# Performance work log

Measured on AMD Instinct MI355X. Metric: run time of the kernel, lower is better.

The kernel has to match this reference:

```python
import jax, jax.numpy as jnp
import numpy as np
from functools import partial

B, S, D_IN, H = 8, 2048, 1024, 1024
V = 50257
NUM_CODEWORDS, EMB_DIM = 256, 16
NUM_NEURONS, TOP_K = 64, 16  # top_k = sparsity(0.25) * 64
TILE_ROWS = 16
NUM_TILES = H // TILE_ROWS  # 64 -> decoder out_features = 1024
FREQS = (1.0, 2.0, 4.0)
MAX_LEN = 1024


def setup_inputs() -> dict:
    key = jax.random.key(0)
    ks = jax.random.split(key, 16)
    s = 0.02
    return {
        "inputs": jax.random.normal(ks[0], (B, S, D_IN), jnp.float32),
        "Wt": jax.random.normal(ks[1], (H, D_IN), jnp.float32) * s,
        "bt": jnp.zeros((H,), jnp.float32),
        "Wq": jax.random.normal(ks[2], (H, H), jnp.float32) * s,
        "bq": jnp.zeros((H,), jnp.float32),
        "Wk": jax.random.normal(ks[3], (H, H), jnp.float32) * s,
        "bk": jnp.zeros((H,), jnp.float32),
        "Wv": jax.random.normal(ks[4], (H, H), jnp.float32) * s,
        "bv": jnp.zeros((H,), jnp.float32),
        "Wo": jax.random.normal(ks[5], (D_IN, H), jnp.float32) * s,
        "bo": jnp.zeros((D_IN,), jnp.float32),
        "codebook": jax.random.normal(ks[6], (NUM_CODEWORDS, EMB_DIM), jnp.float32) * s,
        "instructions": jax.random.randint(ks[7], (NUM_TILES * TILE_ROWS, D_IN // EMB_DIM), 0, NUM_CODEWORDS),
        "W_lm": jax.random.normal(ks[8], (V, NUM_TILES * TILE_ROWS), jnp.float32) * s,
        "b_lm": jnp.zeros((V,), jnp.float32),
    }


def _positional_bias(seq_len):
    # AttentionBasisSynthesizer: sin/cos atoms at freqs (1,2,4), gains=1, shifts=0
    ang = 2.0 * jnp.pi * jnp.arange(seq_len, dtype=jnp.float32) / MAX_LEN
    bias = jnp.zeros((seq_len,), jnp.float32)
    for f in FREQS:
        bias = bias + jnp.sin(f * ang) + jnp.cos(f * ang)
    return bias  # [S]


def _forward(inputs, Wt, bt, Wq, bq, Wk, bk, Wv, bv, Wo, bo, codebook, instructions, W_lm, b_lm):
    tokens = inputs @ Wt.T + bt                       # [B,S,H]
    q = tokens @ Wq.T + bq
    k = tokens @ Wk.T + bk
    v = tokens @ Wv.T + bv
    # per-step KV-cache loop == causal attention over prefix; vectorize
    scores = jnp.einsum("bqh,bkh->bqk", q, k) / jnp.sqrt(jnp.float32(H))
    scores = scores + _positional_bias(S)[None, None, :]
    i = jnp.arange(S)
    causal = i[:, None] >= i[None, :]                 # [S,S]
    scores = jnp.where(causal[None], scores, -jnp.inf)
    attn = jnp.einsum("bqk,bkh->bqh", jax.nn.softmax(scores, axis=-1), v)  # [B,S,H]
    # sparse routing: group into NUM_NEURONS neurons, keep top-k by L2 norm,
    # softmax weights over kept neurons, straight-through combine with dense path
    g = attn.reshape(B, S, NUM_NEURONS, H // NUM_NEURONS)
    sc = jnp.sqrt(jnp.sum(g * g, axis=-1))            # [B,S,N]
    vals, idx = jax.lax.top_k(sc, TOP_K)              # [B,S,K]
    w = jax.nn.softmax(vals, axis=-1)
    onehot = jax.nn.one_hot(idx, NUM_NEURONS, dtype=attn.dtype)  # [B,S,K,N]
    wfull = jnp.einsum("bsk,bskn->bsn", w, onehot)    # [B,S,N]
    combined = (g * wfull[..., None]).reshape(B, S, H)
    combined = combined + (attn - jax.lax.stop_gradient(attn))  # straight-through
    dec_in = combined @ Wo.T + bo                     # [B,S,D_IN]
    x = jnp.mean(dec_in, axis=1)                      # [B,D_IN]
    # DemopackDecoder: weight rows assembled from codebook via instruction indices
    W_dec = codebook[instructions].reshape(NUM_TILES * TILE_ROWS, D_IN)
    hidden = x @ W_dec.T                              # [B, 1024]
    return hidden @ W_lm.T + b_lm                     # [B, V]


def reference(inputs, Wt, bt, Wq, bq, Wk, bk, Wv, bv, Wo, bo, codebook, instructions, W_lm, b_lm):
    return _forward(inputs, Wt, bt, Wq, bq, Wk, bk, Wv, bv, Wo, bo, codebook, instructions, W_lm, b_lm)
```

## Files before the change

### kernel.cpp

```cpp
#include <hip/hip_runtime.h>
#include <cstdint>
#include <cstddef>

#define B_   8
#define S_   2048
#define DIN_ 1024
#define H_   1024
#define V_   50257

typedef unsigned short ushort_t;
typedef __bf16 bf16x8 __attribute__((ext_vector_type(8)));
typedef float  f32x4  __attribute__((ext_vector_type(4)));

__device__ __forceinline__ ushort_t f2bf(float x) {
    unsigned u = __float_as_uint(x);
    u = (u + 0x7fffu + ((u >> 16) & 1u)) >> 16;
    return (ushort_t)u;
}

__device__ __forceinline__ void async16(const void* g, void* s) {
    __builtin_amdgcn_global_load_lds(
        (const __attribute__((address_space(1))) unsigned int*)g,
        (__attribute__((address_space(3))) unsigned int*)s, 16, 0, 0);
}

__device__ __forceinline__ float wredmax(float v) {
#pragma unroll
    for (int o = 32; o; o >>= 1) v = fmaxf(v, __shfl_xor(v, o));
    return v;
}
__device__ __forceinline__ float wredsum(float v) {
#pragma unroll
    for (int o = 32; o; o >>= 1) v += __shfl_xor(v, o);
    return v;
}

#define NB0 16384
#define NB1 19456
#define NB2 19712
#define NB3 20480
#define NB4 20488
__global__ __launch_bounds__(256)
void setup_all(const float* __restrict__ inputs,
               const float* __restrict__ Wq, const float* __restrict__ Wk,
               const float* __restrict__ Wv, const float* __restrict__ Wt,
               const float* __restrict__ bq, const float* __restrict__ bk,
               const float* __restrict__ bv, const float* __restrict__ bt,
               ushort_t* __restrict__ inbf, ushort_t* __restrict__ wqkv_bf,
               ushort_t* __restrict__ wtT, float* __restrict__ bcomb,
               float* __restrict__ pbias) {
    __shared__ float twt[64][65];
    int blk = blockIdx.x, tid = threadIdx.x;
    if (blk < NB0) {
        int i = blk * 256 + tid;
        float4 f = ((const float4*)inputs)[i];
        ushort4 u;
        u.x = f2bf(f.x); u.y = f2bf(f.y); u.z = f2bf(f.z); u.w = f2bf(f.w);
        ((ushort4*)inbf)[i] = u;
    } else if (blk < NB1) {
        int i = (blk - NB0) * 256 + tid;
        int w = i >> 18, off = i & 262143;
        const float* src = w == 0 ? Wq : (w == 1 ? Wk : Wv);
        float4 f = ((const float4*)src)[off];
        ushort4 u;
        u.x = f2bf(f.x); u.y = f2bf(f.y); u.z = f2bf(f.z); u.w = f2bf(f.w);
        ((ushort4*)(wqkv_bf + (size_t)w * 1048576))[off] = u;
    } else if (blk < NB2) {
        int j = blk - NB1;
        int k0 = (j & 15) * 64, i0 = (j >> 4) * 64;
        int tx = tid & 63, ty = tid >> 6;
#pragma unroll
        for (int jj = 0; jj < 16; jj++) {
            int k = ty * 16 + jj;
            twt[k][tx] = Wt[(size_t)(k0 + k) * DIN_ + i0 + tx];
        }
        __syncthreads();
#pragma unroll
        for (int jj = 0; jj < 16; jj++) {
            int i = ty * 16 + jj;
            wtT[(size_t)(i0 + i) * H_ + k0 + tx] = f2bf(twt[tx][i]);
        }
    } else if (blk < NB3) {
        int wave = tid >> 6, lane = tid & 63;
        int j = (blk - NB2) * 4 + wave;
        const float* W  = j < 1024 ? Wq : (j < 2048 ? Wk : Wv);
        const float* bb = j < 1024 ? bq : (j < 2048 ? bk : bv);
        int rowj = j & 1023;
        const float4* wr4 = (const float4*)(W + (size_t)rowj * 1024);
        const float4* bt4 = (const float4*)bt;
        float s = 0.f;
#pragma unroll
        for (int c = 0; c < 4; c++) {
            float4 w = wr4[c * 64 + lane];
            float4 b = bt4[c * 64 + lane];
            s += w.x * b.x + w.y * b.y + w.z * b.z + w.w * b.w;
        }
        s = wredsum(s);
        if (lane == 0) bcomb[j] = s + bb[rowj];
    } else {
        int k = (blk - NB3) * 256 + tid;
        float ang = 6.283185307179586f * (float)k / 1024.0f;
        float b = 0.f;
        b += sinf(1.f * ang) + cosf(1.f * ang);
        b += sinf(2.f * ang) + cosf(2.f * ang);
        b += sinf(4.f * ang) + cosf(4.f * ang);
        pbias[k] = b;
    }
}

template <int OUT_BF16>
__global__ __launch_bounds__(256)
void gemm_bt(const ushort_t* __restrict__ A, int lda,
             const ushort_t* __restrict__ Bt, int ldb,
             void* __restrict__ Cv, int ldc, int K, const float* __restrict__ bias) {
    int bn = blockIdx.x, bm = blockIdx.y;
    __shared__ ushort_t As[128 * 32];
    __shared__ ushort_t Bs[128 * 32];
    int tid = threadIdx.x, wave = tid >> 6, lane = tid & 63;
    int wr = wave >> 1, wc = wave & 1;
    int nkt = K >> 5;
    int srow = lane >> 2, scol = (lane & 3) * 8;
    size_t arow0 = (size_t)bm * 128, brow0 = (size_t)bn * 128;
    f32x4 acc[4][4];
#pragma unroll
    for (int m = 0; m < 4; m++)
#pragma unroll
        for (int n = 0; n < 4; n++) acc[m][n] = f32x4{0.f, 0.f, 0.f, 0.f};
    for (int kt = 0; kt < nkt; ++kt) {
        int k0 = kt * 32;
#pragma unroll
        for (int i = 0; i < 2; i++) {
            int reg = wave * 2 + i;
            int row = reg * 16 + srow;
            async16(A + (arow0 + row) * (size_t)lda + k0 + scol, (ushort_t*)As + reg * 512);
            async16(Bt + (brow0 + row) * (size_t)ldb + k0 + scol, (ushort_t*)Bs + reg * 512);
        }
        __syncthreads();
        bf16x8 af[4], bfr[4];
#pragma unroll
        for (int m = 0; m < 4; m++)
            af[m] = *(const bf16x8*)&As[(wr * 64 + m * 16 + (lane & 15)) * 32 + (lane >> 4) * 8];
#pragma unroll
        for (int n = 0; n < 4; n++)
            bfr[n] = *(const bf16x8*)&Bs[(wc * 64 + n * 16 + (lane & 15)) * 32 + (lane >> 4) * 8];
#pragma unroll
        for (int m = 0; m < 4; m++)
#pragma unroll
            for (int n = 0; n < 4; n++)
                acc[m][n] = __builtin_amdgcn_mfma_f32_16x16x32_bf16(af[m], bfr[n], acc[m][n], 0, 0, 0);
        __syncthreads();
    }
    int rl = (lane >> 4) * 4, cl = lane & 15;
#pragma unroll
    for (int m = 0; m < 4; m++)
#pragma unroll
        for (int n = 0; n < 4; n++) {
            int col = bn * 128 + wc * 64 + n * 16 + cl;
            float badd = bias ? bias[col] : 0.f;
#pragma unroll
            for (int r = 0; r < 4; r++) {
                int row = bm * 128 + wr * 64 + m * 16 + rl + r;
                float v = acc[m][n][r] + badd;
                size_t off = (size_t)row * ldc + col;
                if (OUT_BF16) ((ushort_t*)Cv)[off] = f2bf(v);
                else          ((float*)Cv)[off] = v;
            }
        }
}

template <int OUT_BF16, int MODE>
__global__ __launch_bounds__(512, 2)
void gemm256(const ushort_t* __restrict__ A, size_t sAb, int lda,
             const ushort_t* __restrict__ Bt, size_t sBb, int ldb,
             void* __restrict__ Cv, size_t sCb, int ldc,
             int K, const float* __restrict__ bias, int nbn, int nwg,
             float* __restrict__ Cv2) {
    extern __shared__ char lds[];
    int bz = blockIdx.y;
    int bm, bn, koff = 0, nkt;
    void* Cuse = Cv;
    size_t sCuse = sCb;
    if (MODE == 2) {
        int x = blockIdx.x;
        if (x < 32) {
            bm = x >> 2; bn = x & 3;
            int km = (bm + 1) * 256; if (km > 1024) km = 1024;
            nkt = km >> 6;
        } else {
            int j = x - 32;
            bm = 7 - (j >> 2); bn = j & 3;
            koff = 1024;
            nkt = ((bm + 1) * 256 - 1024) >> 6;
            Cuse = Cv2;
            sCuse = (size_t)1024 * 1024;
        }
    } else if (MODE == 1) {
        int orig = blockIdx.x;
        if (orig >= 36) {
            ushort_t (*t)[66] = (ushort_t(*)[66])lds;
            ushort_t* vT = (ushort_t*)Cv2;
            const ushort_t* qkvp = A;
            int j = orig - 36;
            int tx = threadIdx.x & 63, ty = threadIdx.x >> 6;
            for (int rep = 0; rep < 8; rep++) {
                int tile = j * 8 + rep;
                int s0 = (tile & 31) * 64, h0 = (tile >> 5) * 64;
#pragma unroll
                for (int i = 0; i < 8; i++) {
                    int s = ty * 8 + i;
                    t[s][tx] = qkvp[((size_t)bz * S_ + s0 + s) * 3072 + 2048 + h0 + tx];
                }
                __syncthreads();
#pragma unroll
                for (int i = 0; i < 8; i++) {
                    int h = ty * 8 + i;
                    vT[((size_t)bz * H_ + h0 + h) * S_ + s0 + tx] = t[tx][h];
                }
                __syncthreads();
            }
            return;
        }
        int qq = 36 >> 3, rr8 = 36 & 7;
        int xcd = orig & 7, bidx = orig >> 3;
        int wgid = (xcd < rr8 ? xcd * (qq + 1) : rr8 * (qq + 1) + (xcd - rr8) * qq) + bidx;
        int w = wgid;
        bm = 0;
        while ((bm + 1) * (bm + 2) / 2 <= w) bm++;
        bn = w - bm * (bm + 1) / 2;
        nkt = K >> 6;
    } else {
        int orig = blockIdx.x;
        int qq = nwg >> 3, rr8 = nwg & 7;
        int xcd = orig & 7, bidx = orig >> 3;
        int wgid = (xcd < rr8 ? xcd * (qq + 1) : rr8 * (qq + 1) + (xcd - rr8) * qq) + bidx;
        bm = wgid / nbn; bn = wgid - bm * nbn;
        nkt = K >> 6;
    }

    const ushort_t* Ab = A + (size_t)bz * sAb;
    const ushort_t* Bb = Bt + (size_t)bz * sBb;
    int tid = threadIdx.x, wave = tid >> 6, lane = tid & 63;
    int wr = wave >> 2, wc = wave & 3;

    int srow = wave * 8 + (lane >> 3);
    int sswz = ((lane & 7) ^ (lane >> 3)) * 8;
    const ushort_t* Ag = Ab + ((size_t)bm * 256 + srow) * (size_t)lda + sswz + koff;
    const ushort_t* Bg = Bb + ((size_t)bn * 256 + srow) * (size_t)ldb + sswz + koff;
    int sdst = wave * 1024;

    int fr = lane & 15, g = lane >> 4;
    int kx = (fr >> 2) & 1;
    int gsw = (g ^ (fr & 3)) * 16;
    int aoff = wr * 16384 + fr * 128 + gsw;
    int boff = 32768 + (wc >> 1) * 16384 + ((wc & 1) * 64 + fr) * 128 + gsw;
    int ks0 = kx << 6, ks1 = (kx ^ 1) << 6;

    f32x4 acc[8][4];
#pragma unroll
    for (int m = 0; m < 8; m++)
#pragma unroll
        for (int n = 0; n < 4; n++) acc[m][n] = f32x4{0.f, 0.f, 0.f, 0.f};

#define STG_A(t, h, bo)                                                        \
    do {                                                                       \
        async16(Ag + (size_t)((h) * 128) * lda + (t) * 64,                     \
                lds + (bo) + (h) * 16384 + sdst);                              \
        async16(Ag + (size_t)((h) * 128 + 64) * lda + (t) * 64,                \
                lds + (bo) + (h) * 16384 + 8192 + sdst);                       \
    } while (0)
#define STG_B(t, h, bo)                                                        \
    do {                                                                       \
        async16(Bg + (size_t)((h) * 128) * ldb + (t) * 64,                     \
                lds + (bo) + 32768 + (h) * 16384 + sdst);                      \
        async16(Bg + (size_t)((h) * 128 + 64) * ldb + (t) * 64,                \
                lds + (bo) + 32768 + (h) * 16384 + 8192 + sdst);               \
    } while (0)

    STG_A(0, 0, 0); STG_A(0, 1, 0); STG_B(0, 0, 0); STG_B(0, 1, 0);
    STG_A(1, 0, 65536); STG_A(1, 1, 65536); STG_B(1, 0, 65536); STG_B(1, 1, 65536);
    asm volatile("s_waitcnt vmcnt(8)" ::: "memory");
    __builtin_amdgcn_sched_barrier(0);
    __builtin_amdgcn_s_barrier();
    __builtin_amdgcn_sched_barrier(0);

    bf16x8 af03[4][2], af47[4][2], bf01[2][2], bf23[2][2];
#pragma unroll
    for (int mf = 0; mf < 4; mf++) {
        af03[mf][0] = *(const bf16x8*)(lds + aoff + mf * 2048 + ks0);
        af03[mf][1] = *(const bf16x8*)(lds + aoff + mf * 2048 + ks1);
    }
#pragma unroll
    for (int nf = 0; nf < 2; nf++) {
        bf01[nf][0] = *(const bf16x8*)(lds + boff + nf * 2048 + ks0);
        bf01[nf][1] = *(const bf16x8*)(lds + boff + nf * 2048 + ks1);
    }

    int bufo = 0;
    for (int t = 0; t < nkt; ++t, bufo ^= 65536) {
        int nb = bufo ^ 65536;
#pragma unroll
        for (int mf = 0; mf < 4; mf++) {
            af47[mf][0] = *(const bf16x8*)(lds + bufo + aoff + (mf + 4) * 2048 + ks0);
            af47[mf][1] = *(const bf16x8*)(lds + bufo + aoff + (mf + 4) * 2048 + ks1);
        }
        __builtin_amdgcn_s_setprio(1);
#pragma unroll
        for (int mf = 0; mf < 4; mf++)
#pragma unroll
            for (int nf = 0; nf < 2; nf++) {
                acc[mf][nf] = __builtin_amdgcn_mfma_f32_16x16x32_bf16(af03[mf][0], bf01[nf][0], acc[mf][nf], 0, 0, 0);
                acc[mf][nf] = __builtin_amdgcn_mfma_f32_16x16x32_bf16(af03[mf][1], bf01[nf][1], acc[mf][nf], 0, 0, 0);
            }
        __builtin_amdgcn_s_setprio(0);
        __builtin_amdgcn_sched_barrier(0);
        asm volatile("s_waitcnt lgkmcnt(0)" ::: "memory");
        __builtin_amdgcn_sched_barrier(0);
        __builtin_amdgcn_s_barrier();
        __builtin_amdgcn_sched_barrier(0);

#pragma unroll
        for (int nf = 0; nf < 2; nf++) {
            bf23[nf][0] = *(const bf16x8*)(lds + bufo + boff + (nf + 2) * 2048 + ks0);
            bf23[nf][1] = *(const bf16x8*)(lds + bufo + boff + (nf + 2) * 2048 + ks1);
        }
        __builtin_amdgcn_s_setprio(1);
#pragma unroll
        for (int mf = 0; mf < 4; mf++)
#pragma unroll
            for (int nf = 0; nf < 2; nf++) {
                acc[mf + 4][nf] = __builtin_amdgcn_mfma_f32_16x16x32_bf16(af47[mf][0], bf01[nf][0], acc[mf + 4][nf], 0, 0, 0);
                acc[mf + 4][nf] = __builtin_amdgcn_mfma_f32_16x16x32_bf16(af47[mf][1], bf01[nf][1], acc[mf + 4][nf], 0, 0, 0);
            }
        __builtin_amdgcn_s_setprio(0);
        __builtin_amdgcn_sched_barrier(0);
        __builtin_amdgcn_s_barrier();
        __builtin_amdgcn_sched_barrier(0);

        if (t + 2 < nkt) STG_A(t + 2, 0, bufo);
        __builtin_amdgcn_s_setprio(1);
#pragma unroll
        for (int mf = 0; mf < 4; mf++)
#pragma unroll
            for (int nf = 0; nf < 2; nf++) {
                acc[mf][nf + 2] = __builtin_amdgcn_mfma_f32_16x16x32_bf16(af03[mf][0], bf23[nf][0], acc[mf][nf + 2], 0, 0, 0);
                acc[mf][nf + 2] = __builtin_amdgcn_mfma_f32_16x16x32_bf16(af03[mf][1], bf23[nf][1], acc[mf][nf + 2], 0, 0, 0);
            }
        __builtin_amdgcn_s_setprio(0);
        __builtin_amdgcn_sched_barrier(0);
        if (t + 1 < nkt) {
            if (t + 2 < nkt) { asm volatile("s_waitcnt vmcnt(2)" ::: "memory"); }
            else             { asm volatile("s_waitcnt vmcnt(0)" ::: "memory"); }
        }
        __builtin_amdgcn_s_barrier();
        __builtin_amdgcn_sched_barrier(0);

        if (t + 1 < nkt) {
#pragma unroll
            for (int mf = 0; mf < 4; mf++) {
                af03[mf][0] = *(const bf16x8*)(lds + nb + aoff + mf * 2048 + ks0);
                af03[mf][1] = *(const bf16x8*)(lds + nb + aoff + mf * 2048 + ks1);
            }
#pragma unroll
            for (int nf = 0; nf < 2; nf++) {
                bf01[nf][0] = *(const bf16x8*)(lds + nb + boff + nf * 2048 + ks0);
                bf01[nf][1] = *(const bf16x8*)(lds + nb + boff + nf * 2048 + ks1);
            }
        }
        if (t + 2 < nkt) { STG_A(t + 2, 1, bufo); STG_B(t + 2, 0, bufo); STG_B(t + 2, 1, bufo); }
        __builtin_amdgcn_s_setprio(1);
#pragma unroll
        for (int mf = 0; mf < 4; mf++)
#pragma unroll
            for (int nf = 0; nf < 2; nf++) {
                acc[mf + 4][nf + 2] = __builtin_amdgcn_mfma_f32_16x16x32_bf16(af47[mf][0], bf23[nf][0], acc[mf + 4][nf + 2], 0, 0, 0);
                acc[mf + 4][nf + 2] = __builtin_amdgcn_mfma_f32_16x16x32_bf16(af47[mf][1], bf23[nf][1], acc[mf + 4][nf + 2], 0, 0, 0);
            }
        __builtin_amdgcn_s_setprio(0);
        __builtin_amdgcn_sched_barrier(0);
        __builtin_amdgcn_s_barrier();
        __builtin_amdgcn_sched_barrier(0);
    }
#undef STG_A
#undef STG_B

    int rl = (lane >> 4) * 4, cl = lane & 15;
#pragma unroll
    for (int mf = 0; mf < 8; mf++)
#pragma unroll
        for (int nf = 0; nf < 4; nf++) {
            int col = bn * 256 + wc * 64 + nf * 16 + cl;
            float badd = bias ? bias[col] : 0.f;
#pragma unroll
            for (int r = 0; r < 4; r++) {
                int row = bm * 256 + wr * 128 + mf * 16 + rl + r;
                float v = acc[mf][nf][r] + badd;
                size_t off = (size_t)bz * sCuse + (size_t)row * ldc + col;
                if (OUT_BF16) ((ushort_t*)Cuse)[off] = f2bf(v);
                else          ((float*)Cuse)[off] = v;
            }
        }
}

__global__ __launch_bounds__(256)
void softmax_kernel(const float* __restrict__ scores, ushort_t* __restrict__ P,
                    const float* __restrict__ bias) {
    __shared__ float red[8];
    int q = blockIdx.x, b = blockIdx.y;
    int L = q + 1;
    int tid = threadIdx.x;
    const float4* srow4 = (const float4*)(scores + ((size_t)b * S_ + q) * S_);
    const float4* bias4 = (const float4*)bias;
    const float scale = 0.03125f;
    int kz = ((q >> 8) + 1) * 256;

    int k00 = tid * 4, k01 = 1024 + tid * 4;
    float4 v0 = {0.f, 0.f, 0.f, 0.f}, v1 = {0.f, 0.f, 0.f, 0.f};
    float lm = -3e38f;
    if (k00 < kz) {
        float4 s4 = srow4[tid];
        float4 b4 = bias4[tid];
        v0.x = (k00 + 0 < L) ? s4.x * scale + b4.x : -3e38f;
        v0.y = (k00 + 1 < L) ? s4.y * scale + b4.y : -3e38f;
        v0.z = (k00 + 2 < L) ? s4.z * scale + b4.z : -3e38f;
        v0.w = (k00 + 3 < L) ? s4.w * scale + b4.w : -3e38f;
        lm = fmaxf(fmaxf(v0.x, v0.y), fmaxf(v0.z, v0.w));
    }
    if (k01 < kz) {
        float4 s4 = srow4[256 + tid];
        float4 b4 = bias4[256 + tid];
        v1.x = (k01 + 0 < L) ? s4.x * scale + b4.x : -3e38f;
        v1.y = (k01 + 1 < L) ? s4.y * scale + b4.y : -3e38f;
        v1.z = (k01 + 2 < L) ? s4.z * scale + b4.z : -3e38f;
        v1.w = (k01 + 3 < L) ? s4.w * scale + b4.w : -3e38f;
        lm = fmaxf(lm, fmaxf(fmaxf(v1.x, v1.y), fmaxf(v1.z, v1.w)));
    }
    lm = wredmax(lm);
    if ((tid & 63) == 0) red[tid >> 6] = lm;
    __syncthreads();
    float m = fmaxf(fmaxf(red[0], red[1]), fmaxf(red[2], red[3]));

    float ls = 0.f;
    if (k00 < kz) {
        v0.x = __expf(v0.x - m); v0.y = __expf(v0.y - m);
        v0.z = __expf(v0.z - m); v0.w = __expf(v0.w - m);
        ls += v0.x + v0.y + v0.z + v0.w;
    }
    if (k01 < kz) {
        v1.x = __expf(v1.x - m); v1.y = __expf(v1.y - m);
        v1.z = __expf(v1.z - m); v1.w = __expf(v1.w - m);
        ls += v1.x + v1.y + v1.z + v1.w;
    }
    ls = wredsum(ls);
    if ((tid & 63) == 0) red[4 + (tid >> 6)] = ls;
    __syncthreads();
    float invs = 1.f / (red[4] + red[5] + red[6] + red[7]);

    ushort_t* prow = P + ((size_t)b * S_ + q) * S_;
    if (k00 < kz) {
        ushort4 o;
        o.x = f2bf(v0.x * invs); o.y = f2bf(v0.y * invs);
        o.z = f2bf(v0.z * invs); o.w = f2bf(v0.w * invs);
        ((ushort4*)prow)[tid] = o;
    }
    if (k01 < kz) {
        ushort4 o;
        o.x = f2bf(v1.x * invs); o.y = f2bf(v1.y * invs);
        o.z = f2bf(v1.z * invs); o.w = f2bf(v1.w * invs);
        ((ushort4*)prow)[256 + tid] = o;
    }
}

__global__ __launch_bounds__(256)
void routing_kernel(const float* __restrict__ attn, const float* __restrict__ attn2,
                    ushort_t* __restrict__ combined) {
    int wave = threadIdx.x >> 6, lane = threadIdx.x & 63;
    size_t row = (size_t)blockIdx.x * 4 + wave;
    const float4* a4 = (const float4*)(attn + row * H_);
    float4 x0 = a4[lane * 4 + 0], x1 = a4[lane * 4 + 1];
    float4 x2 = a4[lane * 4 + 2], x3 = a4[lane * 4 + 3];
    int q = (int)(row & 2047);
    if (q >= 1024) {
        size_t b = row >> 11;
        const float4* a2 = (const float4*)(attn2 + ((b * 1024 + (size_t)(q - 1024)) * H_));
        float4 y0 = a2[lane * 4 + 0], y1 = a2[lane * 4 + 1];
        float4 y2 = a2[lane * 4 + 2], y3 = a2[lane * 4 + 3];
        x0.x += y0.x; x0.y += y0.y; x0.z += y0.z; x0.w += y0.w;
        x1.x += y1.x; x1.y += y1.y; x1.z += y1.z; x1.w += y1.w;
        x2.x += y2.x; x2.y += y2.y; x2.z += y2.z; x2.w += y2.w;
        x3.x += y3.x; x3.y += y3.y; x3.z += y3.z; x3.w += y3.w;
    }
    float ss = x0.x * x0.x + x0.y * x0.y + x0.z * x0.z + x0.w * x0.w
             + x1.x * x1.x + x1.y * x1.y + x1.z * x1.z + x1.w * x1.w
             + x2.x * x2.x + x2.y * x2.y + x2.z * x2.z + x2.w * x2.w
             + x3.x * x3.x + x3.y * x3.y + x3.z * x3.z + x3.w * x3.w;
    float sc = sqrtf(ss);

    float v = sc, thr = 0.f, mx = 0.f;
#pragma unroll
    for (int i = 0; i < 16; i++) {
        float mm = wredmax(v);
        if (i == 0) mx = mm;
        thr = mm;
        if (v == mm) v = -1e30f;
    }
    float e = (sc >= thr) ? __expf(sc - mx) : 0.f;
    float se = wredsum(e);
    float w = e / se;

    const float xs[16] = {x0.x, x0.y, x0.z, x0.w, x1.x, x1.y, x1.z, x1.w,
                          x2.x, x2.y, x2.z, x2.w, x3.x, x3.y, x3.z, x3.w};
    union { ushort_t u[16]; uint4 q4[2]; } pk;
#pragma unroll
    for (int j = 0; j < 16; j++) pk.u[j] = f2bf(xs[j] * w);
    uint4* dst = (uint4*)(combined + row * H_ + lane * 16);
    dst[0] = pk.q4[0];
    dst[1] = pk.q4[1];
}

__global__ void cmean_part(const ushort_t* __restrict__ comb, float* __restrict__ part) {
    int d = blockIdx.x * 256 + threadIdx.x;
    int sc = blockIdx.y, b = blockIdx.z;
    const ushort_t* p = comb + ((size_t)b * S_ + sc * 128) * H_ + d;
    float s = 0.f;
    for (int i = 0; i < 128; i++) s += __uint_as_float((unsigned)p[(size_t)i * H_] << 16);
    part[((size_t)b * 16 + sc) * H_ + d] = s;
}

__global__ void cmean_final(const float* __restrict__ part, float* __restrict__ cm) {
    int idx = blockIdx.x * 256 + threadIdx.x;
    int b = idx >> 10, d = idx & 1023;
    float s = 0.f;
#pragma unroll
    for (int c = 0; c < 16; c++) s += part[((size_t)b * 16 + c) * DIN_ + d];
    cm[idx] = s * (1.0f / 2048.0f);
}

__global__ __launch_bounds__(256)
void xgemv(const float* __restrict__ cm, const float* __restrict__ Wo,
           const float* __restrict__ bo, float* __restrict__ x) {
    int wave = threadIdx.x >> 6, lane = threadIdx.x & 63;
    int i = blockIdx.x * 4 + wave;
    const float4* wr4 = (const float4*)(Wo + (size_t)i * H_);
    float4 w[4];
#pragma unroll
    for (int c = 0; c < 4; c++) w[c] = wr4[c * 64 + lane];
    float accv[B_];
#pragma unroll
    for (int b = 0; b < B_; b++) {
        const float4* c4 = (const float4*)(cm + (size_t)b * H_);
        float s = 0.f;
#pragma unroll
        for (int c = 0; c < 4; c++) {
            float4 h = c4[c * 64 + lane];
            s += w[c].x * h.x + w[c].y * h.y + w[c].z * h.z + w[c].w * h.w;
        }
        accv[b] = wredsum(s);
    }
    if (lane == 0) {
        float bi = bo[i];
#pragma unroll
        for (int b = 0; b < B_; b++) x[(size_t)b * DIN_ + i] = accv[b] + bi;
    }
}

__global__ __launch_bounds__(64)
void decode_hidden(const float* __restrict__ x, const float* __restrict__ codebook,
                   const int* __restrict__ instr, float* __restrict__ hidden) {
    int r = blockIdx.x;
    int lane = threadIdx.x;
    int idx = instr[r * 64 + lane];
    const float4* cw = (const float4*)(codebook + (size_t)idx * 16);
    float4 c0 = cw[0], c1 = cw[1], c2 = cw[2], c3 = cw[3];
    float acc[B_];
#pragma unroll
    for (int b = 0; b < B_; b++) {
        const float4* xb = (const float4*)(x + (size_t)b * DIN_ + lane * 16);
        float4 h0 = xb[0], h1 = xb[1], h2 = xb[2], h3 = xb[3];
        acc[b] = c0.x * h0.x + c0.y * h0.y + c0.z * h0.z + c0.w * h0.w
               + c1.x * h1.x + c1.y * h1.y + c1.z * h1.z + c1.w * h1.w
               + c2.x * h2.x + c2.y * h2.y + c2.z * h2.z + c2.w * h2.w
               + c3.x * h3.x + c3.y * h3.y + c3.z * h3.z + c3.w * h3.w;
    }
#pragma unroll
    for (int b = 0; b < B_; b++) acc[b] = wredsum(acc[b]);
    if (lane == 0) {
#pragma unroll
        for (int b = 0; b < B_; b++) hidden[(size_t)b * 1024 + r] = acc[b];
    }
}

__global__ __launch_bounds__(256)
void lm_head(const float* __restrict__ Wlm, const float* __restrict__ hidden,
             const float* __restrict__ blm, float* __restrict__ out) {
    int wave = threadIdx.x >> 6, lane = threadIdx.x & 63;
    for (int v = blockIdx.x * 4 + wave; v < V_; v += gridDim.x * 4) {
        const float4* wrow = (const float4*)(Wlm + (size_t)v * 1024);
        float acc[B_];
#pragma unroll
        for (int b = 0; b < B_; b++) acc[b] = 0.f;
#pragma unroll
        for (int rr = 0; rr < 4; rr++) {
            float4 wv = wrow[rr * 64 + lane];
#pragma unroll
            for (int b = 0; b < B_; b++) {
                float4 hv = ((const float4*)hidden)[b * 256 + rr * 64 + lane];
                acc[b] += wv.x * hv.x + wv.y * hv.y + wv.z * hv.z + wv.w * hv.w;
            }
        }
#pragma unroll
        for (int b = 0; b < B_; b++) acc[b] = wredsum(acc[b]);
        if (lane == 0) {
            float bl = blm[v];
#pragma unroll
            for (int b = 0; b < B_; b++) out[(size_t)b * V_ + v] = acc[b] + bl;
        }
    }
}

extern "C" void kernel_launch(void* const* d_in, const int* in_sizes, int n_in,
                              void* d_out, int out_size, void* d_ws, size_t ws_size,
                              hipStream_t stream) {
    const float* inputs = (const float*)d_in[0];
    const float* Wt  = (const float*)d_in[1];
    const float* bt  = (const float*)d_in[2];
    const float* Wq  = (const float*)d_in[3];
    const float* bq  = (const float*)d_in[4];
    const float* Wk  = (const float*)d_in[5];
    const float* bk  = (const float*)d_in[6];
    const float* Wv  = (const float*)d_in[7];
    const float* bv  = (const float*)d_in[8];
    const float* Wo  = (const float*)d_in[9];
    const float* bo  = (const float*)d_in[10];
    const float* codebook = (const float*)d_in[11];
    const int*   instructions = (const int*)d_in[12];
    const float* Wlm = (const float*)d_in[13];
    const float* blm = (const float*)d_in[14];
    float* out = (float*)d_out;

    (void)hipFuncSetAttribute(reinterpret_cast<const void*>(&gemm256<1, 0>),
                              hipFuncAttributeMaxDynamicSharedMemorySize, 131072);
    (void)hipFuncSetAttribute(reinterpret_cast<const void*>(&gemm256<0, 1>),
                              hipFuncAttributeMaxDynamicSharedMemorySize, 131072);
    (void)hipFuncSetAttribute(reinterpret_cast<const void*>(&gemm256<0, 2>),
                              hipFuncAttributeMaxDynamicSharedMemorySize, 131072);

    const size_t MB = 1024 * 1024;
    char* ws = (char*)d_ws;
    ushort_t* wqkv_bf = (ushort_t*)(ws + 0);
    ushort_t* wtT_bf  = (ushort_t*)(ws + 6 * MB);
    ushort_t* wcomb   = (ushort_t*)(ws + 8 * MB);
    float* bcomb  = (float*)(ws + 14 * MB);
    float* pbias  = (float*)(ws + 14 * MB + 64 * 1024);
    float* cm     = (float*)(ws + 14 * MB + 128 * 1024);
    float* xbuf   = (float*)(ws + 14 * MB + 192 * 1024);
    float* hidden = (float*)(ws + 14 * MB + 256 * 1024);
    float* part   = (float*)(ws + 14 * MB + 512 * 1024);
    ushort_t* inbf   = (ushort_t*)(ws + 16 * MB);
    ushort_t* qkv    = (ushort_t*)(ws + 48 * MB);
    ushort_t* vT     = (ushort_t*)(ws + 144 * MB);
    float* scores    = (float*)(ws + 176 * MB);
    ushort_t* P      = (ushort_t*)(ws + 304 * MB);
    float* attn      = (float*)(ws + 48 * MB);
    float* attn2     = (float*)(ws + 112 * MB);
    ushort_t* combined = (ushort_t*)(ws + 176 * MB);

    setup_all<<<NB4, 256, 0, stream>>>(inputs, Wq, Wk, Wv, Wt, bq, bk, bv, bt,
                                       inbf, wqkv_bf, wtT_bf, bcomb, pbias);

    gemm_bt<1><<<dim3(8, 24), 256, 0, stream>>>(wqkv_bf, 1024, wtT_bf, 1024,
                                                wcomb, 1024, 1024, nullptr);

    gemm256<1, 0><<<dim3(768, 1), 512, 131072, stream>>>(
        inbf, 0, 1024, wcomb, 0, 1024, qkv, 0, 3072, 1024, bcomb, 12, 768, nullptr);

    gemm256<0, 1><<<dim3(100, 8), 512, 131072, stream>>>(
        qkv, (size_t)S_ * 3072, 3072, qkv + 1024, (size_t)S_ * 3072, 3072,
        scores, (size_t)S_ * S_, S_, 1024, nullptr, 36, 36, (float*)vT);

    softmax_kernel<<<dim3(S_, B_), 256, 0, stream>>>(scores, P, pbias);

    gemm256<0, 2><<<dim3(48, 8), 512, 131072, stream>>>(
        P, (size_t)S_ * S_, S_, vT, (size_t)H_ * S_, S_,
        attn, (size_t)S_ * H_, H_, S_, nullptr, 0, 0, attn2 - (size_t)1024 * 1024);

    routing_kernel<<<4096, 256, 0, stream>>>(attn, attn2, combined);

    cmean_part<<<dim3(4, 16, 8), 256, 0, stream>>>(combined, part);
    cmean_final<<<32, 256, 0, stream>>>(part, cm);
    xgemv<<<256, 256, 0, stream>>>(cm, Wo, bo, xbuf);

    decode_hidden<<<1024, 64, 0, stream>>>(xbuf, codebook, instructions, hidden);

    lm_head<<<2048, 256, 0, stream>>>(Wlm, hidden, blm, out);
}
```

Measured before the change: 433.5 us.

## Halve GEMM K-tile to 32 to cut LDS to 64KB, vectorize cmean

The main 256x256 GEMM kernel now uses a K-step of 32 instead of 64 per iteration. That halves the double-buffered LDS footprint from 128KB to 64KB, and the swizzle, staging addresses and wait counts are reworked to match. The smaller footprint lets more workgroups fit per CU, which should improve occupancy and latency hiding. The cost is twice as many loop iterations and barriers per tile, with less MFMA work between barriers. Separately, the column-mean partial kernel now has each thread load 4 bf16 values at once, using a quarter of the blocks.

Result: slower. 464.6 us (+7.2%).

```diff
diff --git a/kernel.cpp b/kernel.cpp
--- a/kernel.cpp
+++ b/kernel.cpp
@@ -16,6 +16,9 @@
     unsigned u = __float_as_uint(x);
     u = (u + 0x7fffu + ((u >> 16) & 1u)) >> 16;
     return (ushort_t)u;
+}
+__device__ __forceinline__ float bf2f(ushort_t x) {
+    return __uint_as_float((unsigned)x << 16);
 }
 
 __device__ __forceinline__ void async16(const void* g, void* s) {
@@ -185,12 +188,12 @@
         if (x < 32) {
             bm = x >> 2; bn = x & 3;
             int km = (bm + 1) * 256; if (km > 1024) km = 1024;
-            nkt = km >> 6;
+            nkt = km >> 5;
         } else {
             int j = x - 32;
             bm = 7 - (j >> 2); bn = j & 3;
             koff = 1024;
-            nkt = ((bm + 1) * 256 - 1024) >> 6;
+            nkt = ((bm + 1) * 256 - 1024) >> 5;
             Cuse = Cv2;
             sCuse = (size_t)1024 * 1024;
         }
@@ -227,14 +230,14 @@
         bm = 0;
         while ((bm + 1) * (bm + 2) / 2 <= w) bm++;
         bn = w - bm * (bm + 1) / 2;
-        nkt = K >> 6;
+        nkt = K >> 5;
     } else {
         int orig = blockIdx.x;
         int qq = nwg >> 3, rr8 = nwg & 7;
         int xcd = orig & 7, bidx = orig >> 3;
         int wgid = (xcd < rr8 ? xcd * (qq + 1) : rr8 * (qq + 1) + (xcd - rr8) * qq) + bidx;
         bm = wgid / nbn; bn = wgid - bm * nbn;
-        nkt = K >> 6;
+        nkt = K >> 5;
     }
 
     const ushort_t* Ab = A + (size_t)bz * sAb;
@@ -242,18 +245,16 @@
     int tid = threadIdx.x, wave = tid >> 6, lane = tid & 63;
     int wr = wave >> 2, wc = wave & 3;
 
-    int srow = wave * 8 + (lane >> 3);
-    int sswz = ((lane & 7) ^ (lane >> 3)) * 8;
+    int srow = wave * 16 + (lane >> 2);
+    int sswz = ((lane & 3) ^ ((lane >> 2) & 3)) * 8;
     const ushort_t* Ag = Ab + ((size_t)bm * 256 + srow) * (size_t)lda + sswz + koff;
     const ushort_t* Bg = Bb + ((size_t)bn * 256 + srow) * (size_t)ldb + sswz + koff;
     int sdst = wave * 1024;
 
     int fr = lane & 15, g = lane >> 4;
-    int kx = (fr >> 2) & 1;
-    int gsw = (g ^ (fr & 3)) * 16;
-    int aoff = wr * 16384 + fr * 128 + gsw;
-    int boff = 32768 + (wc >> 1) * 16384 + ((wc & 1) * 64 + fr) * 128 + gsw;
-    int ks0 = kx << 6, ks1 = (kx ^ 1) << 6;
+    int gsw = (g ^ (fr & 3)) << 4;
+    int aoff = (wr * 128 + fr) * 64 + gsw;
+    int boff = 16384 + (wc * 64 + fr) * 64 + gsw;
 
     f32x4 acc[8][4];
 #pragma unroll
@@ -262,55 +263,39 @@
         for (int n = 0; n < 4; n++) acc[m][n] = f32x4{0.f, 0.f, 0.f, 0.f};
 
 #define STG_A(t, h, bo)                                                        \
-    do {                                                                       \
-        async16(Ag + (size_t)((h) * 128) * lda + (t) * 64,                     \
-                lds + (bo) + (h) * 16384 + sdst);                              \
-        async16(Ag + (size_t)((h) * 128 + 64) * lda + (t) * 64,                \
-                lds + (bo) + (h) * 16384 + 8192 + sdst);                       \
-    } while (0)
+    async16(Ag + (size_t)((h) * 128) * lda + (t) * 32,                         \
+            lds + (bo) + (h) * 8192 + sdst)
 #define STG_B(t, h, bo)                                                        \
-    do {                                                                       \
-        async16(Bg + (size_t)((h) * 128) * ldb + (t) * 64,                     \
-                lds + (bo) + 32768 + (h) * 16384 + sdst);                      \
-        async16(Bg + (size_t)((h) * 128 + 64) * ldb + (t) * 64,                \
-                lds + (bo) + 32768 + (h) * 16384 + 8192 + sdst);               \
-    } while (0)
+    async16(Bg + (size_t)((h) * 128) * ldb + (t) * 32,                         \
+            lds + (bo) + 16384 + (h) * 8192 + sdst)
 
     STG_A(0, 0, 0); STG_A(0, 1, 0); STG_B(0, 0, 0); STG_B(0, 1, 0);
-    STG_A(1, 0, 65536); STG_A(1, 1, 65536); STG_B(1, 0, 65536); STG_B(1, 1, 65536);
-    asm volatile("s_waitcnt vmcnt(8)" ::: "memory");
+    STG_A(1, 0, 32768); STG_A(1, 1, 32768); STG_B(1, 0, 32768); STG_B(1, 1, 32768);
+    asm volatile("s_waitcnt vmcnt(4)" ::: "memory");
     __builtin_amdgcn_sched_barrier(0);
     __builtin_amdgcn_s_barrier();
     __builtin_amdgcn_sched_barrier(0);
 
-    bf16x8 af03[4][2], af47[4][2], bf01[2][2], bf23[2][2];
-#pragma unroll
-    for (int mf = 0; mf < 4; mf++) {
-        af03[mf][0] = *(const bf16x8*)(lds + aoff + mf * 2048 + ks0);
-        af03[mf][1] = *(const bf16x8*)(lds + aoff + mf * 2048 + ks1);
-    }
-#pragma unroll
-    for (int nf = 0; nf < 2; nf++) {
-        bf01[nf][0] = *(const bf16x8*)(lds + boff + nf * 2048 + ks0);
-        bf01[nf][1] = *(const bf16x8*)(lds + boff + nf * 2048 + ks1);
-    }
+    bf16x8 af03[4], af47[4], bf01[2], bf23[2];
+#pragma unroll
+    for (int mf = 0; mf < 4; mf++)
+        af03[mf] = *(const bf16x8*)(lds + aoff + mf * 1024);
+#pragma unroll
+    for (int nf = 0; nf < 2; nf++)
+        bf01[nf] = *(const bf16x8*)(lds + boff + nf * 1024);
 
     int bufo = 0;
-    for (int t = 0; t < nkt; ++t, bufo ^= 65536) {
-        int nb = bufo ^ 65536;
-#pragma unroll
-        for (int mf = 0; mf < 4; mf++) {
-            af47[mf][0] = *(const bf16x8*)(lds + bufo + aoff + (mf + 4) * 2048 + ks0);
-            af47[mf][1] = *(const bf16x8*)(lds + bufo + aoff + (mf + 4) * 2048 + ks1);
-        }
+    for (int t = 0; t < nkt; ++t, bufo ^= 32768) {
+        int nb = bufo ^ 32768;
+#pragma unroll
+        for (int mf = 0; mf < 4; mf++)
+            af47[mf] = *(const bf16x8*)(lds + bufo + aoff + (mf + 4) * 1024);
         __builtin_amdgcn_s_setprio(1);
 #pragma unroll
         for (int mf = 0; mf < 4; mf++)
 #pragma unroll
-            for (int nf = 0; nf < 2; nf++) {
-                acc[mf][nf] = __builtin_amdgcn_mfma_f32_16x16x32_bf16(af03[mf][0], bf01[nf][0], acc[mf][nf], 0, 0, 0);
-                acc[mf][nf] = __builtin_amdgcn_mfma_f32_16x16x32_bf16(af03[mf][1], bf01[nf][1], acc[mf][nf], 0, 0, 0);
-            }
+            for (int nf = 0; nf < 2; nf++)
+                acc[mf][nf] = __builtin_amdgcn_mfma_f32_16x16x32_bf16(af03[mf], bf01[nf], acc[mf][nf], 0, 0, 0);
         __builtin_amdgcn_s_setprio(0);
         __builtin_amdgcn_sched_barrier(0);
         asm volatile("s_waitcnt lgkmcnt(0)" ::: "memory");
@@ -319,18 +304,14 @@
         __builtin_amdgcn_sched_barrier(0);
 
 #pragma unroll
-        for (int nf = 0; nf < 2; nf++) {
-            bf23[nf][0] = *(const bf16x8*)(lds + bufo + boff + (nf + 2) * 2048 + ks0);
-            bf23[nf][1] = *(const bf16x8*)(lds + bufo + boff + (nf + 2) * 2048 + ks1);
-        }
+        for (int nf = 0; nf < 2; nf++)
+            bf23[nf] = *(const bf16x8*)(lds + bufo + boff + (nf + 2) * 1024);
         __builtin_amdgcn_s_setprio(1);
 #pragma unroll
         for (int mf = 0; mf < 4; mf++)
 #pragma unroll
-            for (int nf = 0; nf < 2; nf++) {
-                acc[mf + 4][nf] = __builtin_amdgcn_mfma_f32_16x16x32_bf16(af47[mf][0], bf01[nf][0], acc[mf + 4][nf], 0, 0, 0);
-                acc[mf + 4][nf] = __builtin_amdgcn_mfma_f32_16x16x32_bf16(af47[mf][1], bf01[nf][1], acc[mf + 4][nf], 0, 0, 0);
-            }
+            for (int nf = 0; nf < 2; nf++)
+                acc[mf + 4][nf] = __builtin_amdgcn_mfma_f32_16x16x32_bf16(af47[mf], bf01[nf], acc[mf + 4][nf], 0, 0, 0);
         __builtin_amdgcn_s_setprio(0);
         __builtin_amdgcn_sched_barrier(0);
         __builtin_amdgcn_s_barrier();
@@ -341,14 +322,12 @@
 #pragma unroll
         for (int mf = 0; mf < 4; mf++)
 #pragma unroll
-            for (int nf = 0; nf < 2; nf++) {
-                acc[mf][nf + 2] = __builtin_amdgcn_mfma_f32_16x16x32_bf16(af03[mf][0], bf23[nf][0], acc[mf][nf + 2], 0, 0, 0);
-                acc[mf][nf + 2] = __builtin_amdgcn_mfma_f32_16x16x32_bf16(af03[mf][1], bf23[nf][1], acc[mf][nf + 2], 0, 0, 0);
-            }
+            for (int nf = 0; nf < 2; nf++)
+                acc[mf][nf + 2] = __builtin_amdgcn_mfma_f32_16x16x32_bf16(af03[mf], bf23[nf], acc[mf][nf + 2], 0, 0, 0);
         __builtin_amdgcn_s_setprio(0);
         __builtin_amdgcn_sched_barrier(0);
         if (t + 1 < nkt) {
-            if (t + 2 < nkt) { asm volatile("s_waitcnt vmcnt(2)" ::: "memory"); }
+            if (t + 2 < nkt) { asm volatile("s_waitcnt vmcnt(1)" ::: "memory"); }
             else             { asm volatile("s_waitcnt vmcnt(0)" ::: "memory"); }
         }
         __builtin_amdgcn_s_barrier();
@@ -356,25 +335,19 @@
 
         if (t + 1 < nkt) {
 #pragma unroll
-            for (int mf = 0; mf < 4; mf++) {
-                af03[mf][0] = *(const bf16x8*)(lds + nb + aoff + mf * 2048 + ks0);
-                af03[mf][1] = *(const bf16x8*)(lds + nb + aoff + mf * 2048 + ks1);
-            }
-#pragma unroll
-            for (int nf = 0; nf < 2; nf++) {
-                bf01[nf][0] = *(const bf16x8*)(lds + nb + boff + nf * 2048 + ks0);
-                bf01[nf][1] = *(const bf16x8*)(lds + nb + boff + nf * 2048 + ks1);
-            }
+            for (int mf = 0; mf < 4; mf++)
+                af03[mf] = *(const bf16x8*)(lds + nb + aoff + mf * 1024);
+#pragma unroll
+            for (int nf = 0; nf < 2; nf++)
+                bf01[nf] = *(const bf16x8*)(lds + nb + boff + nf * 1024);
         }
         if (t + 2 < nkt) { STG_A(t + 2, 1, bufo); STG_B(t + 2, 0, bufo); STG_B(t + 2, 1, bufo); }
         __builtin_amdgcn_s_setprio(1);
 #pragma unroll
         for (int mf = 0; mf < 4; mf++)
 #pragma unroll
-            for (int nf = 0; nf < 2; nf++) {
-                acc[mf + 4][nf + 2] = __builtin_amdgcn_mfma_f32_16x16x32_bf16(af47[mf][0], bf23[nf][0], acc[mf + 4][nf + 2], 0, 0, 0);
-                acc[mf + 4][nf + 2] = __builtin_amdgcn_mfma_f32_16x16x32_bf16(af47[mf][1], bf23[nf][1], acc[mf + 4][nf + 2], 0, 0, 0);
-            }
+            for (int nf = 0; nf < 2; nf++)
+                acc[mf + 4][nf + 2] = __builtin_amdgcn_mfma_f32_16x16x32_bf16(af47[mf], bf23[nf], acc[mf + 4][nf + 2], 0, 0, 0);
         __builtin_amdgcn_s_setprio(0);
         __builtin_amdgcn_sched_barrier(0);
         __builtin_amdgcn_s_barrier();
@@ -518,12 +491,15 @@
 }
 
 __global__ void cmean_part(const ushort_t* __restrict__ comb, float* __restrict__ part) {
-    int d = blockIdx.x * 256 + threadIdx.x;
+    int tid = threadIdx.x;
     int sc = blockIdx.y, b = blockIdx.z;
-    const ushort_t* p = comb + ((size_t)b * S_ + sc * 128) * H_ + d;
-    float s = 0.f;
-    for (int i = 0; i < 128; i++) s += __uint_as_float((unsigned)p[(size_t)i * H_] << 16);
-    part[((size_t)b * 16 + sc) * H_ + d] = s;
+    const ushort_t* p = comb + ((size_t)b * S_ + sc * 128) * H_ + tid * 4;
+    float4 s = {0.f, 0.f, 0.f, 0.f};
+    for (int i = 0; i < 128; i++) {
+        ushort4 v = *(const ushort4*)(p + (size_t)i * H_);
+        s.x += bf2f(v.x); s.y += bf2f(v.y); s.z += bf2f(v.z); s.w += bf2f(v.w);
+    }
+    ((float4*)(part + ((size_t)b * 16 + sc) * H_))[tid] = s;
 }
 
 __global__ void cmean_final(const float* __restrict__ part, float* __restrict__ cm) {
@@ -638,11 +614,11 @@
     float* out = (float*)d_out;
 
     (void)hipFuncSetAttribute(reinterpret_cast<const void*>(&gemm256<1, 0>),
-                              hipFuncAttributeMaxDynamicSharedMemorySize, 131072);
+                              hipFuncAttributeMaxDynamicSharedMemorySize, 65536);
     (void)hipFuncSetAttribute(reinterpret_cast<const void*>(&gemm256<0, 1>),
-                              hipFuncAttributeMaxDynamicSharedMemorySize, 131072);
+                              hipFuncAttributeMaxDynamicSharedMemorySize, 65536);
     (void)hipFuncSetAttribute(reinterpret_cast<const void*>(&gemm256<0, 2>),
-                              hipFuncAttributeMaxDynamicSharedMemorySize, 131072);
+                              hipFuncAttributeMaxDynamicSharedMemorySize, 65536);
 
     const size_t MB = 1024 * 1024;
     char* ws = (char*)d_ws;
@@ -670,22 +646,22 @@
     gemm_bt<1><<<dim3(8, 24), 256, 0, stream>>>(wqkv_bf, 1024, wtT_bf, 1024,
                                                 wcomb, 1024, 1024, nullptr);
 
-    gemm256<1, 0><<<dim3(768, 1), 512, 131072, stream>>>(
+    gemm256<1, 0><<<dim3(768, 1), 512, 65536, stream>>>(
         inbf, 0, 1024, wcomb, 0, 1024, qkv, 0, 3072, 1024, bcomb, 12, 768, nullptr);
 
-    gemm256<0, 1><<<dim3(100, 8), 512, 131072, stream>>>(
+    gemm256<0, 1><<<dim3(100, 8), 512, 65536, stream>>>(
         qkv, (size_t)S_ * 3072, 3072, qkv + 1024, (size_t)S_ * 3072, 3072,
         scores, (size_t)S_ * S_, S_, 1024, nullptr, 36, 36, (float*)vT);
 
     softmax_kernel<<<dim3(S_, B_), 256, 0, stream>>>(scores, P, pbias);
 
-    gemm256<0, 2><<<dim3(48, 8), 512, 131072, stream>>>(
+    gemm256<0, 2><<<dim3(48, 8), 512, 65536, stream>>>(
         P, (size_t)S_ * S_, S_, vT, (size_t)H_ * S_, S_,
         attn, (size_t)S_ * H_, H_, S_, nullptr, 0, 0, attn2 - (size_t)1024 * 1024);
 
     routing_kernel<<<4096, 256, 0, stream>>>(attn, attn2, combined);
 
-    cmean_part<<<dim3(4, 16, 8), 256, 0, stream>>>(combined, part);
+    cmean_part<<<dim3(1, 16, 8), 256, 0, stream>>>(combined, part);
     cmean_final<<<32, 256, 0, stream>>>(part, cm);
     xgemv<<<256, 256, 0, stream>>>(cm, Wo, bo, xbuf);
 
```
